# Optimization experiments

Measured on AMD Instinct MI355X. Metric: run time of the kernel, lower is better.

## Reference

```python
import jax, jax.numpy as jnp
import numpy as np

N_USERS = 50000
N_ITEMS = 30000
NNZ = 1_600_000
EMBED = 128
ATT = 128
TAU = 0.5


def setup_inputs() -> dict:
    key = jax.random.key(0)
    ks = jax.random.split(key, 9)
    user_embed = jax.random.normal(ks[0], (N_USERS, EMBED), dtype=jnp.float32)
    item_embed = jax.random.normal(ks[1], (N_ITEMS, EMBED), dtype=jnp.float32)
    Wq = jax.random.normal(ks[2], (ATT, EMBED), dtype=jnp.float32) * (1.0 / np.sqrt(EMBED))
    bq = jnp.zeros((ATT,), dtype=jnp.float32)
    Wk = jax.random.normal(ks[3], (ATT, EMBED), dtype=jnp.float32) * (1.0 / np.sqrt(EMBED))
    bk = jnp.zeros((ATT,), dtype=jnp.float32)
    adj_vals = jnp.ones((NNZ,), dtype=jnp.float32)
    gumbel_u_ui = jax.random.uniform(ks[4], (NNZ,), dtype=jnp.float32, minval=1e-10, maxval=1.0)
    gumbel_u_iu = jax.random.uniform(ks[5], (NNZ,), dtype=jnp.float32, minval=1e-10, maxval=1.0)
    rows = jax.random.randint(ks[6], (NNZ,), 0, N_USERS, dtype=jnp.int32)
    cols = jax.random.randint(ks[7], (NNZ,), 0, N_ITEMS, dtype=jnp.int32)
    return dict(user_embed=user_embed, item_embed=item_embed, Wq=Wq, bq=bq, Wk=Wk, bk=bk,
                adj_vals=adj_vals, gumbel_u_ui=gumbel_u_ui, gumbel_u_iu=gumbel_u_iu,
                rows=rows, cols=cols)


def _segment_softmax(vals, seg, num_segments):
    # numerically stable softmax over edges grouped by segment id (sparse row softmax)
    m = jax.ops.segment_max(vals, seg, num_segments=num_segments)
    e = jnp.exp(vals - m[seg])
    s = jax.ops.segment_sum(e, seg, num_segments=num_segments)
    return e / s[seg]


def reference(user_embed, item_embed, Wq, bq, Wk, bk, adj_vals, gumbel_u_ui, gumbel_u_iu, rows, cols):
    # ---- M_ui = sparse_softmax_rows( (adj * (Q(u) @ K(i).T) - G) / tau ) on edge support ----
    Qu = user_embed @ Wq.T + bq          # [U, A]
    Ki = item_embed @ Wk.T + bk          # [I, A]
    # edge-wise dot: equals dense (Qu @ Ki.T)[rows, cols] without materializing [U, I]
    w_ui = adj_vals * jnp.einsum('ed,ed->e', Qu[rows], Ki[cols])
    g_ui = jnp.log(-jnp.log(gumbel_u_ui))
    ui_vals = _segment_softmax((w_ui - g_ui) / TAU, rows, N_USERS)
    # ---- M_iu: transpose adjacency, Q over items, K over users, row-softmax over items ----
    Qi = item_embed @ Wq.T + bq          # [I, A]
    Ku = user_embed @ Wk.T + bk          # [U, A]
    w_iu = adj_vals * jnp.einsum('ed,ed->e', Qi[cols], Ku[rows])
    g_iu = jnp.log(-jnp.log(gumbel_u_iu))
    iu_vals = _segment_softmax((w_iu - g_iu) / TAU, cols, N_ITEMS)
    # block mask [[0, M_ui], [M_iu, 0]]: pads contribute nothing, so the nonzero
    # values of the concatenated mask are exactly these two edge-value arrays.
    return jnp.stack([ui_vals, iu_vals])  # [2, NNZ]
```

## Files before the change

### kernel.cpp

```cpp
#include <hip/hip_runtime.h>
#include <hip/hip_bf16.h>


#define EMB 128
#define TAUINV 2.0f
#define LOG2E 1.44269504f

__device__ __forceinline__ unsigned fkey(float f) {
    unsigned u = __float_as_uint(f);
    return (u & 0x80000000u) ? ~u : (u | 0x80000000u);
}
__device__ __forceinline__ float fdecode(unsigned u) {
    return __uint_as_float((u & 0x80000000u) ? (u ^ 0x80000000u) : ~u);
}

__device__ __forceinline__ double dexp_fast(float lg) {
    float t = lg * LOG2E;
    float kf = floorf(t);
    float f = exp2f(t - kf);
    return ldexp((double)f, (int)kf);
}

__global__ void k_prep(const float* __restrict__ Wq, const float* __restrict__ Wk,
                       const float* __restrict__ bq, const float* __restrict__ bk,
                       float* __restrict__ BIGM, float* __restrict__ v1,
                       float* __restrict__ v2, float* __restrict__ c0) {
    int e1 = blockIdx.x, e2 = threadIdx.x;
    float acc = 0.f;
    for (int a = 0; a < EMB; ++a) acc += Wq[a * EMB + e1] * Wk[a * EMB + e2];
    BIGM[e2 * 256 + e1] = acc;
    BIGM[e1 * 256 + 128 + e2] = acc;
    if (e2 == 0) { float s = 0.f; for (int a = 0; a < EMB; ++a) s += Wq[a * EMB + e1] * bk[a]; v1[e1] = s; }
    if (e2 == 1) { float s = 0.f; for (int a = 0; a < EMB; ++a) s += Wk[a * EMB + e1] * bq[a]; v2[e1] = s; }
    if (e1 == 0 && e2 == 2) { float s = 0.f; for (int a = 0; a < EMB; ++a) s += bq[a] * bk[a]; *c0 = s; }
}

__global__ __launch_bounds__(256) void k_cd(const float* __restrict__ Xi,
                                            const float* __restrict__ BIGM,
                                            float* __restrict__ CD, int nItems) {
    __shared__ float Xs[32][EMB];
    __shared__ float Ms[32][256];
    const int t = threadIdx.x;
    const int m0 = blockIdx.x * 32;

    const float4* Xi4 = (const float4*)Xi;
    float4* Xs4 = (float4*)Xs;
    for (int idx = t; idx < 32 * 32; idx += 256) {
        int r = idx >> 5, c = idx & 31;
        int row = m0 + r;
        Xs4[idx] = (row < nItems) ? Xi4[(size_t)row * 32 + c]
                                  : make_float4(0.f, 0.f, 0.f, 0.f);
    }

    const int tc = t & 63;
    const int tr = t >> 6;
    float4 acc[8] = {};

    const float4* BG4 = (const float4*)BIGM;
    float4* Ms4 = (float4*)Ms;
    for (int kc = 0; kc < EMB; kc += 32) {
        __syncthreads();
        for (int idx = t; idx < 32 * 64; idx += 256)
            Ms4[idx] = BG4[(size_t)(kc + (idx >> 6)) * 64 + (idx & 63)];
        __syncthreads();
#pragma unroll
        for (int kk = 0; kk < 32; ++kk) {
            float4 w = Ms4[kk * 64 + tc];
#pragma unroll
            for (int i = 0; i < 8; ++i) {
                float x = Xs[tr * 8 + i][kc + kk];
                acc[i].x += x * w.x; acc[i].y += x * w.y;
                acc[i].z += x * w.z; acc[i].w += x * w.w;
            }
        }
    }
#pragma unroll
    for (int i = 0; i < 8; ++i) {
        int row = m0 + tr * 8 + i;
        if (row < nItems)
            ((float4*)(CD + (size_t)row * 256))[tc] = acc[i];
    }
}

__global__ void k_rowdot2(const float* __restrict__ Xu, const float* __restrict__ Xi,
                          int U, int I,
                          const float* __restrict__ v1, const float* __restrict__ v2,
                          float2* __restrict__ t12, float2* __restrict__ u12) {
    int g = blockIdx.x * 8 + (threadIdx.x >> 5);
    int l = threadIdx.x & 31;
    if (g >= U + I) return;
    const float* X = (g < U) ? (Xu + (size_t)g * EMB) : (Xi + (size_t)(g - U) * EMB);
    float4 x = ((const float4*)X)[l];
    float4 av = ((const float4*)v1)[l];
    float4 bv = ((const float4*)v2)[l];
    float pa = x.x * av.x + x.y * av.y + x.z * av.z + x.w * av.w;
    float pb = x.x * bv.x + x.y * bv.y + x.z * bv.z + x.w * bv.w;
    for (int off = 16; off; off >>= 1) { pa += __shfl_xor(pa, off); pb += __shfl_xor(pb, off); }
    if (l == 0) {
        if (g < U) t12[g] = make_float2(pa, pb);
        else       u12[g - U] = make_float2(pb, pa);
    }
}

__global__ void k_hist2(const int* __restrict__ cols, int nnz,
                        unsigned* __restrict__ cnt) {
    int i = blockIdx.x * blockDim.x + threadIdx.x, st = gridDim.x * blockDim.x;
    for (int e = i; e < nnz; e += st) atomicAdd(&cnt[cols[e]], 1u);
}

__global__ void k_scan1(const unsigned* __restrict__ cnt, unsigned* __restrict__ off,
                        unsigned* __restrict__ bsum, int n) {
    __shared__ unsigned sh[256];
    int i = blockIdx.x * 256 + threadIdx.x;
    unsigned v = (i < n) ? cnt[i] : 0u;
    sh[threadIdx.x] = v; __syncthreads();
    for (int d = 1; d < 256; d <<= 1) {
        unsigned t = (threadIdx.x >= d) ? sh[threadIdx.x - d] : 0u; __syncthreads();
        sh[threadIdx.x] += t; __syncthreads();
    }
    if (i < n) off[i] = sh[threadIdx.x] - v;
    if (threadIdx.x == 255) bsum[blockIdx.x] = sh[255];
}

__global__ void k_scan2(unsigned* __restrict__ bsum, int nb) {
    __shared__ unsigned sh[256];
    __shared__ unsigned carry;
    if (threadIdx.x == 0) carry = 0u;
    __syncthreads();
    for (int base = 0; base < nb; base += 256) {
        int i = base + threadIdx.x;
        unsigned v = (i < nb) ? bsum[i] : 0u;
        sh[threadIdx.x] = v; __syncthreads();
        for (int d = 1; d < 256; d <<= 1) {
            unsigned t = (threadIdx.x >= d) ? sh[threadIdx.x - d] : 0u; __syncthreads();
            sh[threadIdx.x] += t; __syncthreads();
        }
        unsigned c = carry;
        if (i < nb) bsum[i] = c + sh[threadIdx.x] - v;
        __syncthreads();
        if (threadIdx.x == 0) carry = c + sh[255];
        __syncthreads();
    }
}

__global__ void k_scan3(unsigned* __restrict__ off, const unsigned* __restrict__ bsum, int n) {
    int i = blockIdx.x * 256 + threadIdx.x;
    if (i < n) off[i] += bsum[blockIdx.x];
}

__global__ void k_scatter7(const int* __restrict__ rows, const int* __restrict__ cols,
                           const float* __restrict__ adj, const float* __restrict__ gu1,
                           const float* __restrict__ gu2,
                           const float2* __restrict__ t12, const float2* __restrict__ u12,
                           const float* __restrict__ c0p, int nnz,
                           unsigned* __restrict__ off, int* __restrict__ S6) {
    const float c0 = *c0p;
    int i = blockIdx.x * blockDim.x + threadIdx.x, st = gridDim.x * blockDim.x;
    for (int e = i; e < nnz; e += st) {
        int r = rows[e], c = cols[e];
        unsigned pos = atomicAdd(&off[c], 1u);
        float a = adj[e];
        float g1 = logf(-logf(gu1[e]));
        float g2 = logf(-logf(gu2[e]));
        float2 tt = t12[r];
        float2 uu = u12[c];
        float b1 = (a * (tt.x + uu.x + c0) - g1) * TAUINV;
        float b2 = (a * (tt.y + uu.y + c0) - g2) * TAUINV;
        int* p = S6 + (size_t)pos * 6;
        *(int2*)(p)     = make_int2(r, e);
        *(int2*)(p + 2) = make_int2(__float_as_int(a * TAUINV), __float_as_int(b1));
        *(int2*)(p + 4) = make_int2(__float_as_int(b2), 0);
    }
}

__global__ __launch_bounds__(256) void k_edge10(
    const float* __restrict__ Xu, const float* __restrict__ CD,
    const unsigned* __restrict__ offp, const int* __restrict__ S6,
    float2* __restrict__ L12, double* __restrict__ s1d, double* __restrict__ s2d,
    int I) {
    const int g = threadIdx.x >> 4, l = threadIdx.x & 15;
    const int c = blockIdx.x * 16 + g;
    if (c >= I) return;
    const unsigned lo = (c == 0) ? 0u : offp[c - 1];
    const unsigned hi = offp[c];
    if (lo >= hi) return;
    const float4* cd = (const float4*)(CD + (size_t)c * 256);
    const float4 cv0 = cd[l], cv1 = cd[l + 16];
    const float4 dv0 = cd[l + 32], dv1 = cd[l + 48];
    double s2acc = 0.0;
    for (unsigned j = lo; j < hi; ++j) {
        const int* sp = S6 + (size_t)j * 6;
        int2 re = *(const int2*)sp;
        int2 ab = *(const int2*)(sp + 2);
        int2 b2p = *(const int2*)(sp + 4);
        const float4* xu = (const float4*)(Xu + (size_t)re.x * EMB);
        float4 x0 = xu[l], x1 = xu[l + 16];
        float p1 = x0.x * cv0.x + x0.y * cv0.y + x0.z * cv0.z + x0.w * cv0.w
                 + x1.x * cv1.x + x1.y * cv1.y + x1.z * cv1.z + x1.w * cv1.w;
        float p2 = x0.x * dv0.x + x0.y * dv0.y + x0.z * dv0.z + x0.w * dv0.w
                 + x1.x * dv1.x + x1.y * dv1.y + x1.z * dv1.z + x1.w * dv1.w;
#pragma unroll
        for (int off = 1; off < 16; off <<= 1) {
            p1 += __shfl_xor(p1, off);
            p2 += __shfl_xor(p2, off);
        }
        if (l < 2) {
            float aP = __int_as_float(ab.x);
            float bP = __int_as_float((l == 0) ? ab.y : b2p.x);
            float lg = fmaf(aP, (l == 0) ? p1 : p2, bP);
            double ev = dexp_fast(lg);
            ((float*)(L12 + re.y))[l] = lg;
            if (l == 0) unsafeAtomicAdd(s1d + re.x, ev);
            else        s2acc += ev;
        }
    }
    if (l == 1) s2d[c] = s2acc;
}

__global__ void k_ls(const double* __restrict__ s1d, const double* __restrict__ s2d,
                     float* __restrict__ ls1, float* __restrict__ ls2, int U, int I) {
    int i = blockIdx.x * blockDim.x + threadIdx.x;
    if (i >= U + I) return;
    double s = (i < U) ? s1d[i] : s2d[i - U];
    int ex;
    double m = frexp(s, &ex);
    float l2 = log2f((float)m) + (float)ex;
    if (i < U) ls1[i] = l2; else ls2[i - U] = l2;
}

__global__ void k_fin4(const int* __restrict__ rows, const int* __restrict__ cols,
                       const float2* __restrict__ L12,
                       const float* __restrict__ ls1, const float* __restrict__ ls2,
                       float* __restrict__ out, int nnz) {
    int i = blockIdx.x * blockDim.x + threadIdx.x, st = gridDim.x * blockDim.x;
    for (int e = i; e < nnz; e += st) {
        float2 lg = L12[e];
        out[e]       = exp2f(fmaf(lg.x, LOG2E, -ls1[rows[e]]));
        out[nnz + e] = exp2f(fmaf(lg.y, LOG2E, -ls2[cols[e]]));
    }
}

__global__ __launch_bounds__(256) void k_edge1(
    const float* __restrict__ Xu, const float* __restrict__ CD,
    const float2* __restrict__ t12, const float2* __restrict__ u12,
    const float* __restrict__ c0p, const float* __restrict__ adj,
    const float* __restrict__ gu1, const float* __restrict__ gu2,
    const int* __restrict__ rows, const int* __restrict__ cols,
    float* __restrict__ L1, float* __restrict__ L2,
    unsigned* __restrict__ mx1, unsigned* __restrict__ mx2, int nnz) {
    const int gid = blockIdx.x * 8 + (threadIdx.x >> 5);
    const int l = threadIdx.x & 31;
    const int stride = gridDim.x * 8;
    const float c0 = *c0p;
    for (int e = gid; e < nnz; e += stride) {
        int r = rows[e], c = cols[e];
        float4 xu = ((const float4*)(Xu + (size_t)r * EMB))[l];
        const float4* cd = (const float4*)(CD + (size_t)c * 256);
        float4 cv = cd[l];
        float4 dv = cd[32 + l];
        float p1 = xu.x * cv.x + xu.y * cv.y + xu.z * cv.z + xu.w * cv.w;
        float p2 = xu.x * dv.x + xu.y * dv.y + xu.z * dv.z + xu.w * dv.w;
        for (int off = 16; off; off >>= 1) { p1 += __shfl_xor(p1, off); p2 += __shfl_xor(p2, off); }
        if (l < 2) {
            float p = (l == 0) ? p1 : p2;
            float2 tt = t12[r];
            float2 uu = u12[c];
            float tb = (l == 0) ? tt.x : tt.y;
            float ub = (l == 0) ? uu.x : uu.y;
            float g = logf(-logf(((l == 0) ? gu1 : gu2)[e]));
            float w = adj[e] * (p + tb + ub + c0);
            float lg = (w - g) * TAUINV;
            if (l == 0) { L1[e] = lg; atomicMax(mx1 + r, fkey(lg)); }
            else        { L2[e] = lg; atomicMax(mx2 + c, fkey(lg)); }
        }
    }
}

__global__ void k_sum(const int* __restrict__ rows, const int* __restrict__ cols,
                      const float* __restrict__ L1, const float* __restrict__ L2,
                      const unsigned* __restrict__ mx1, const unsigned* __restrict__ mx2,
                      float* __restrict__ s1, float* __restrict__ s2, int nnz) {
    int i = blockIdx.x * blockDim.x + threadIdx.x, st = gridDim.x * blockDim.x;
    for (int e = i; e < nnz; e += st) {
        int r = rows[e], c = cols[e];
        atomicAdd(s1 + r, expf(L1[e] - fdecode(mx1[r])));
        atomicAdd(s2 + c, expf(L2[e] - fdecode(mx2[c])));
    }
}

__global__ void k_fin2(const int* __restrict__ rows, const int* __restrict__ cols,
                       const float* __restrict__ L1, const float* __restrict__ L2,
                       const unsigned* __restrict__ mx1, const unsigned* __restrict__ mx2,
                       const float* __restrict__ s1, const float* __restrict__ s2,
                       float* __restrict__ out, int nnz) {
    int i = blockIdx.x * blockDim.x + threadIdx.x, st = gridDim.x * blockDim.x;
    for (int e = i; e < nnz; e += st) {
        int r = rows[e], c = cols[e];
        out[e]       = expf(L1[e] - fdecode(mx1[r])) / s1[r];
        out[nnz + e] = expf(L2[e] - fdecode(mx2[c])) / s2[c];
    }
}

extern "C" void kernel_launch(void* const* d_in, const int* in_sizes, int n_in,
                              void* d_out, int out_size, void* d_ws, size_t ws_size,
                              hipStream_t stream) {
    const float* Xu  = (const float*)d_in[0];
    const float* Xi  = (const float*)d_in[1];
    const float* Wq  = (const float*)d_in[2];
    const float* bq  = (const float*)d_in[3];
    const float* Wk  = (const float*)d_in[4];
    const float* bk  = (const float*)d_in[5];
    const float* adj = (const float*)d_in[6];
    const float* gu1 = (const float*)d_in[7];
    const float* gu2 = (const float*)d_in[8];
    const int* rows  = (const int*)d_in[9];
    const int* cols  = (const int*)d_in[10];
    float* out = (float*)d_out;

    const int U   = in_sizes[0] / EMB;
    const int I   = in_sizes[1] / EMB;
    const int nnz = in_sizes[6];
    const int numB1 = (I + 255) / 256;

    char* w = (char*)d_ws;
    size_t off_b = 0;
    auto alloc = [&](size_t bytes) {
        char* p = w + off_b;
        off_b += (bytes + 15) & ~(size_t)15;
        return p;
    };

    float* BIGM = (float*)alloc(32768 * 4);
    float* v1   = (float*)alloc(128 * 4);
    float* v2   = (float*)alloc(128 * 4);
    float* c0   = (float*)alloc(64 * 4);
    float2* t12 = (float2*)alloc((size_t)U * 8);
    float2* u12 = (float2*)alloc((size_t)I * 8);
    float* CD   = (float*)alloc((size_t)I * 256 * 4);
    float2* L12 = (float2*)alloc((size_t)nnz * 8);
    size_t base_need = off_b;
    double* s1d   = (double*)alloc((size_t)U * 8);
    unsigned* cnt = (unsigned*)alloc((size_t)I * 4);
    double* s2d   = (double*)alloc((size_t)I * 8);
    float* ls1    = (float*)alloc((size_t)U * 4);
    float* ls2    = (float*)alloc((size_t)I * 4);
    unsigned* offp = (unsigned*)alloc((size_t)I * 4);
    unsigned* bsum = (unsigned*)alloc(((size_t)numB1 + 8) * 4);
    int* S6 = (int*)alloc((size_t)nnz * 24);
    size_t sorted_need = off_b;
    unsigned* mx1 = (unsigned*)alloc((size_t)U * 4);
    unsigned* mx2 = (unsigned*)alloc((size_t)I * 4);
    float* s1f  = (float*)alloc((size_t)U * 4);
    float* s2f  = (float*)alloc((size_t)I * 4);
    size_t fallback_need = off_b;

    const bool use_sorted = (sorted_need <= ws_size);
    if (!use_sorted && fallback_need > ws_size) return;

    k_prep<<<128, 128, 0, stream>>>(Wq, Wk, bq, bk, BIGM, v1, v2, c0);
    k_cd<<<(I + 31) / 32, 256, 0, stream>>>(Xi, BIGM, CD, I);
    k_rowdot2<<<(U + I + 7) / 8, 256, 0, stream>>>(Xu, Xi, U, I, v1, v2, t12, u12);

    if (use_sorted) {
        (void)hipMemsetAsync(s1d, 0, (size_t)U * 8 + (size_t)I * 4, stream);
        k_hist2<<<2048, 256, 0, stream>>>(cols, nnz, cnt);
        k_scan1<<<numB1, 256, 0, stream>>>(cnt, offp, bsum, I);
        k_scan2<<<1, 256, 0, stream>>>(bsum, numB1);
        k_scan3<<<numB1, 256, 0, stream>>>(offp, bsum, I);
        k_scatter7<<<2048, 256, 0, stream>>>(rows, cols, adj, gu1, gu2,
                                             t12, u12, c0, nnz, offp, S6);
        k_edge10<<<(I + 15) / 16, 256, 0, stream>>>(Xu, CD, offp, S6, L12,
                                                    s1d, s2d, I);
        k_ls<<<(U + I + 255) / 256, 256, 0, stream>>>(s1d, s2d, ls1, ls2, U, I);
        k_fin4<<<2048, 256, 0, stream>>>(rows, cols, L12, ls1, ls2, out, nnz);
    } else {
        float* L1 = (float*)L12;
        float* L2 = L1 + nnz;
        (void)hipMemsetAsync(mx1, 0, (size_t)(2 * (U + I)) * 4, stream);
        k_edge1<<<4096, 256, 0, stream>>>(Xu, CD, t12, u12, c0, adj, gu1, gu2,
                                          rows, cols, L1, L2, mx1, mx2, nnz);
        k_sum<<<2048, 256, 0, stream>>>(rows, cols, L1, L2, mx1, mx2, s1f, s2f, nnz);
        k_fin2<<<2048, 256, 0, stream>>>(rows, cols, L1, L2, mx1, mx2, s1f, s2f,
                                         out, nnz);
    }
}
```

Measured before the change: 407.2 us.

## Replace counting-sort by column with fixed-capacity per-item buckets plus overflow list

Result: faster. 388.4 us (-4.6%).

```diff
diff --git a/kernel.cpp b/kernel.cpp
--- a/kernel.cpp
+++ b/kernel.cpp
@@ -5,6 +5,8 @@
 #define EMB 128
 #define TAUINV 2.0f
 #define LOG2E 1.44269504f
+#define CAP 128
+#define OCAP 65536
 
 __device__ __forceinline__ unsigned fkey(float f) {
     unsigned u = __float_as_uint(f);
@@ -32,7 +34,8 @@
     BIGM[e1 * 256 + 128 + e2] = acc;
     if (e2 == 0) { float s = 0.f; for (int a = 0; a < EMB; ++a) s += Wq[a * EMB + e1] * bk[a]; v1[e1] = s; }
     if (e2 == 1) { float s = 0.f; for (int a = 0; a < EMB; ++a) s += Wk[a * EMB + e1] * bq[a]; v2[e1] = s; }
-    if (e1 == 0 && e2 == 2) { float s = 0.f; for (int a = 0; a < EMB; ++a) s += bq[a] * bk[a]; *c0 = s; }
+    if (e1 == 0 && e2 == 2) { float s = 0.f; for (int a = 0; a < EMB; ++a) s += bq[a] * bk[a]; c0[0] = s; }
+    if (e1 == 0 && e2 == 3) { float s = 0.f; for (int a = 0; a < EMB; ++a) s += fabsf(bq[a]) + fabsf(bk[a]); c0[1] = s; }
 }
 
 __global__ __launch_bounds__(256) void k_cd(const float* __restrict__ Xi,
@@ -102,98 +105,68 @@
     }
 }
 
-__global__ void k_hist2(const int* __restrict__ cols, int nnz,
-                        unsigned* __restrict__ cnt) {
-    int i = blockIdx.x * blockDim.x + threadIdx.x, st = gridDim.x * blockDim.x;
-    for (int e = i; e < nnz; e += st) atomicAdd(&cnt[cols[e]], 1u);
-}
-
-__global__ void k_scan1(const unsigned* __restrict__ cnt, unsigned* __restrict__ off,
-                        unsigned* __restrict__ bsum, int n) {
-    __shared__ unsigned sh[256];
-    int i = blockIdx.x * 256 + threadIdx.x;
-    unsigned v = (i < n) ? cnt[i] : 0u;
-    sh[threadIdx.x] = v; __syncthreads();
-    for (int d = 1; d < 256; d <<= 1) {
-        unsigned t = (threadIdx.x >= d) ? sh[threadIdx.x - d] : 0u; __syncthreads();
-        sh[threadIdx.x] += t; __syncthreads();
-    }
-    if (i < n) off[i] = sh[threadIdx.x] - v;
-    if (threadIdx.x == 255) bsum[blockIdx.x] = sh[255];
-}
-
-__global__ void k_scan2(unsigned* __restrict__ bsum, int nb) {
-    __shared__ unsigned sh[256];
-    __shared__ unsigned carry;
-    if (threadIdx.x == 0) carry = 0u;
-    __syncthreads();
-    for (int base = 0; base < nb; base += 256) {
-        int i = base + threadIdx.x;
-        unsigned v = (i < nb) ? bsum[i] : 0u;
-        sh[threadIdx.x] = v; __syncthreads();
-        for (int d = 1; d < 256; d <<= 1) {
-            unsigned t = (threadIdx.x >= d) ? sh[threadIdx.x - d] : 0u; __syncthreads();
-            sh[threadIdx.x] += t; __syncthreads();
-        }
-        unsigned c = carry;
-        if (i < nb) bsum[i] = c + sh[threadIdx.x] - v;
-        __syncthreads();
-        if (threadIdx.x == 0) carry = c + sh[255];
-        __syncthreads();
-    }
-}
-
-__global__ void k_scan3(unsigned* __restrict__ off, const unsigned* __restrict__ bsum, int n) {
-    int i = blockIdx.x * 256 + threadIdx.x;
-    if (i < n) off[i] += bsum[blockIdx.x];
-}
-
-__global__ void k_scatter7(const int* __restrict__ rows, const int* __restrict__ cols,
-                           const float* __restrict__ adj, const float* __restrict__ gu1,
-                           const float* __restrict__ gu2,
-                           const float2* __restrict__ t12, const float2* __restrict__ u12,
-                           const float* __restrict__ c0p, int nnz,
-                           unsigned* __restrict__ off, int* __restrict__ S6) {
-    const float c0 = *c0p;
+__global__ void k_scatter_fc(const int* __restrict__ rows, const int* __restrict__ cols,
+                             const float* __restrict__ adj, const float* __restrict__ gu1,
+                             const float* __restrict__ gu2,
+                             const float2* __restrict__ t12, const float2* __restrict__ u12,
+                             const float* __restrict__ c0p, int nnz,
+                             unsigned* __restrict__ cnt, int4* __restrict__ SA,
+                             float* __restrict__ SB, int* __restrict__ OV,
+                             unsigned* __restrict__ ovfc) {
+    const float c0 = c0p[0];
+    const bool useb = (c0p[1] != 0.f);
     int i = blockIdx.x * blockDim.x + threadIdx.x, st = gridDim.x * blockDim.x;
     for (int e = i; e < nnz; e += st) {
         int r = rows[e], c = cols[e];
-        unsigned pos = atomicAdd(&off[c], 1u);
+        unsigned pos = atomicAdd(&cnt[c], 1u);
         float a = adj[e];
         float g1 = logf(-logf(gu1[e]));
         float g2 = logf(-logf(gu2[e]));
-        float2 tt = t12[r];
-        float2 uu = u12[c];
-        float b1 = (a * (tt.x + uu.x + c0) - g1) * TAUINV;
-        float b2 = (a * (tt.y + uu.y + c0) - g2) * TAUINV;
-        int* p = S6 + (size_t)pos * 6;
-        *(int2*)(p)     = make_int2(r, e);
-        *(int2*)(p + 2) = make_int2(__float_as_int(a * TAUINV), __float_as_int(b1));
-        *(int2*)(p + 4) = make_int2(__float_as_int(b2), 0);
-    }
-}
-
-__global__ __launch_bounds__(256) void k_edge10(
+        float b1 = -g1 * TAUINV;
+        float b2 = -g2 * TAUINV;
+        if (useb) {
+            float2 tt = t12[r];
+            float2 uu = u12[c];
+            b1 += a * (tt.x + uu.x + c0) * TAUINV;
+            b2 += a * (tt.y + uu.y + c0) * TAUINV;
+        }
+        if (pos < CAP) {
+            size_t s = (size_t)c * CAP + pos;
+            SA[s] = make_int4(r, e, __float_as_int(a * TAUINV), __float_as_int(b1));
+            SB[s] = b2;
+        } else {
+            unsigned o = atomicAdd(ovfc, 1u);
+            if (o < OCAP) {
+                int* p = OV + (size_t)o * 6;
+                p[0] = r; p[1] = c; p[2] = e;
+                p[3] = __float_as_int(a * TAUINV);
+                p[4] = __float_as_int(b1); p[5] = __float_as_int(b2);
+            }
+        }
+    }
+}
+
+__global__ __launch_bounds__(256) void k_edge14(
     const float* __restrict__ Xu, const float* __restrict__ CD,
-    const unsigned* __restrict__ offp, const int* __restrict__ S6,
+    const unsigned* __restrict__ cnt, const int4* __restrict__ SA,
+    const float* __restrict__ SB,
     float2* __restrict__ L12, double* __restrict__ s1d, double* __restrict__ s2d,
     int I) {
     const int g = threadIdx.x >> 4, l = threadIdx.x & 15;
     const int c = blockIdx.x * 16 + g;
     if (c >= I) return;
-    const unsigned lo = (c == 0) ? 0u : offp[c - 1];
-    const unsigned hi = offp[c];
-    if (lo >= hi) return;
+    unsigned n = cnt[c]; if (n > CAP) n = CAP;
+    if (n == 0) return;
+    const unsigned lo = (unsigned)c * CAP;
+    const unsigned hi = lo + n;
     const float4* cd = (const float4*)(CD + (size_t)c * 256);
     const float4 cv0 = cd[l], cv1 = cd[l + 16];
     const float4 dv0 = cd[l + 32], dv1 = cd[l + 48];
     double s2acc = 0.0;
     for (unsigned j = lo; j < hi; ++j) {
-        const int* sp = S6 + (size_t)j * 6;
-        int2 re = *(const int2*)sp;
-        int2 ab = *(const int2*)(sp + 2);
-        int2 b2p = *(const int2*)(sp + 4);
-        const float4* xu = (const float4*)(Xu + (size_t)re.x * EMB);
+        int4 m = SA[j];
+        float b2s = SB[j];
+        const float4* xu = (const float4*)(Xu + (size_t)m.x * EMB);
         float4 x0 = xu[l], x1 = xu[l + 16];
         float p1 = x0.x * cv0.x + x0.y * cv0.y + x0.z * cv0.z + x0.w * cv0.w
                  + x1.x * cv1.x + x1.y * cv1.y + x1.z * cv1.z + x1.w * cv1.w;
@@ -205,16 +178,54 @@
             p2 += __shfl_xor(p2, off);
         }
         if (l < 2) {
-            float aP = __int_as_float(ab.x);
-            float bP = __int_as_float((l == 0) ? ab.y : b2p.x);
+            float aP = __int_as_float(m.z);
+            float bP = (l == 0) ? __int_as_float(m.w) : b2s;
             float lg = fmaf(aP, (l == 0) ? p1 : p2, bP);
             double ev = dexp_fast(lg);
-            ((float*)(L12 + re.y))[l] = lg;
-            if (l == 0) unsafeAtomicAdd(s1d + re.x, ev);
+            ((float*)(L12 + m.y))[l] = lg;
+            if (l == 0) unsafeAtomicAdd(s1d + m.x, ev);
             else        s2acc += ev;
         }
     }
     if (l == 1) s2d[c] = s2acc;
+}
+
+__global__ void k_ovf(const float* __restrict__ Xu, const float* __restrict__ CD,
+                      const int* __restrict__ OV, const unsigned* __restrict__ ovfc,
+                      float2* __restrict__ L12, double* __restrict__ s1d,
+                      double* __restrict__ s2d) {
+    int n = (int)*ovfc; if (n > OCAP) n = OCAP;
+    if (n == 0) return;
+    const int gid = (blockIdx.x * blockDim.x + threadIdx.x) >> 4;
+    const int ng = (gridDim.x * blockDim.x) >> 4;
+    const int l = threadIdx.x & 15;
+    for (int i = gid; i < n; i += ng) {
+        const int* p = OV + (size_t)i * 6;
+        int r = p[0], c = p[1], e = p[2];
+        const float4* xu = (const float4*)(Xu + (size_t)r * EMB);
+        const float4* cd = (const float4*)(CD + (size_t)c * 256);
+        float4 x0 = xu[l], x1 = xu[l + 16];
+        float4 cv0 = cd[l], cv1 = cd[l + 16];
+        float4 dv0 = cd[l + 32], dv1 = cd[l + 48];
+        float p1 = x0.x * cv0.x + x0.y * cv0.y + x0.z * cv0.z + x0.w * cv0.w
+                 + x1.x * cv1.x + x1.y * cv1.y + x1.z * cv1.z + x1.w * cv1.w;
+        float p2 = x0.x * dv0.x + x0.y * dv0.y + x0.z * dv0.z + x0.w * dv0.w
+                 + x1.x * dv1.x + x1.y * dv1.y + x1.z * dv1.z + x1.w * dv1.w;
+#pragma unroll
+        for (int off = 1; off < 16; off <<= 1) {
+            p1 += __shfl_xor(p1, off);
+            p2 += __shfl_xor(p2, off);
+        }
+        if (l < 2) {
+            float aP = __int_as_float(p[3]);
+            float bP = __int_as_float((l == 0) ? p[4] : p[5]);
+            float lg = fmaf(aP, (l == 0) ? p1 : p2, bP);
+            double ev = dexp_fast(lg);
+            ((float*)(L12 + e))[l] = lg;
+            if (l == 0) unsafeAtomicAdd(s1d + r, ev);
+            else        unsafeAtomicAdd(s2d + c, ev);
+        }
+    }
 }
 
 __global__ void k_ls(const double* __restrict__ s1d, const double* __restrict__ s2d,
@@ -251,7 +262,7 @@
     const int gid = blockIdx.x * 8 + (threadIdx.x >> 5);
     const int l = threadIdx.x & 31;
     const int stride = gridDim.x * 8;
-    const float c0 = *c0p;
+    const float c0 = c0p[0];
     for (int e = gid; e < nnz; e += stride) {
         int r = rows[e], c = cols[e];
         float4 xu = ((const float4*)(Xu + (size_t)r * EMB))[l];
@@ -320,7 +331,6 @@
     const int U   = in_sizes[0] / EMB;
     const int I   = in_sizes[1] / EMB;
     const int nnz = in_sizes[6];
-    const int numB1 = (I + 255) / 256;
 
     char* w = (char*)d_ws;
     size_t off_b = 0;
@@ -339,14 +349,15 @@
     float* CD   = (float*)alloc((size_t)I * 256 * 4);
     float2* L12 = (float2*)alloc((size_t)nnz * 8);
     size_t base_need = off_b;
-    double* s1d   = (double*)alloc((size_t)U * 8);
-    unsigned* cnt = (unsigned*)alloc((size_t)I * 4);
-    double* s2d   = (double*)alloc((size_t)I * 8);
-    float* ls1    = (float*)alloc((size_t)U * 4);
-    float* ls2    = (float*)alloc((size_t)I * 4);
-    unsigned* offp = (unsigned*)alloc((size_t)I * 4);
-    unsigned* bsum = (unsigned*)alloc(((size_t)numB1 + 8) * 4);
-    int* S6 = (int*)alloc((size_t)nnz * 24);
+    double* s1d    = (double*)alloc((size_t)U * 8);
+    unsigned* cnt  = (unsigned*)alloc((size_t)I * 4);
+    unsigned* ovfc = (unsigned*)alloc(16 * 4);
+    double* s2d    = (double*)alloc((size_t)I * 8);
+    float* ls1     = (float*)alloc((size_t)U * 4);
+    float* ls2     = (float*)alloc((size_t)I * 4);
+    int4* SA = (int4*)alloc((size_t)I * CAP * 16);
+    float* SB = (float*)alloc((size_t)I * CAP * 4);
+    int* OV = (int*)alloc((size_t)OCAP * 24);
     size_t sorted_need = off_b;
     unsigned* mx1 = (unsigned*)alloc((size_t)U * 4);
     unsigned* mx2 = (unsigned*)alloc((size_t)I * 4);
@@ -362,15 +373,13 @@
     k_rowdot2<<<(U + I + 7) / 8, 256, 0, stream>>>(Xu, Xi, U, I, v1, v2, t12, u12);
 
     if (use_sorted) {
-        (void)hipMemsetAsync(s1d, 0, (size_t)U * 8 + (size_t)I * 4, stream);
-        k_hist2<<<2048, 256, 0, stream>>>(cols, nnz, cnt);
-        k_scan1<<<numB1, 256, 0, stream>>>(cnt, offp, bsum, I);
-        k_scan2<<<1, 256, 0, stream>>>(bsum, numB1);
-        k_scan3<<<numB1, 256, 0, stream>>>(offp, bsum, I);
-        k_scatter7<<<2048, 256, 0, stream>>>(rows, cols, adj, gu1, gu2,
-                                             t12, u12, c0, nnz, offp, S6);
-        k_edge10<<<(I + 15) / 16, 256, 0, stream>>>(Xu, CD, offp, S6, L12,
+        (void)hipMemsetAsync(s1d, 0, (size_t)U * 8 + (size_t)I * 4 + 64, stream);
+        k_scatter_fc<<<2048, 256, 0, stream>>>(rows, cols, adj, gu1, gu2,
+                                               t12, u12, c0, nnz, cnt, SA, SB,
+                                               OV, ovfc);
+        k_edge14<<<(I + 15) / 16, 256, 0, stream>>>(Xu, CD, cnt, SA, SB, L12,
                                                     s1d, s2d, I);
+        k_ovf<<<64, 256, 0, stream>>>(Xu, CD, OV, ovfc, L12, s1d, s2d);
         k_ls<<<(U + I + 255) / 256, 256, 0, stream>>>(s1d, s2d, ls1, ls2, U, I);
         k_fin4<<<2048, 256, 0, stream>>>(rows, cols, L12, ls1, ls2, out, nnz);
     } else {
```
